# Kernel tuning notes

Measured on AMD Instinct MI355X. Metric: run time of the kernel, lower is better.

## Reference

```python
import jax, jax.numpy as jnp
import numpy as np

D_IN = 2048
D_OUT = 2048
CTX = 2048
N_HEADS = 16
HEAD_DIM = D_OUT // N_HEADS
ROPE_BASE = 10000.0


def precompute_rope(head_dim, context_length, base=ROPE_BASE):
    inv_freq = 1.0 / (base ** (jnp.arange(0, head_dim, 2, dtype=jnp.float32) / head_dim))
    pos = jnp.arange(context_length, dtype=jnp.float32)
    angles = pos[:, None] * inv_freq[None, :]            # (ctx, head_dim/2)
    angles = jnp.concatenate([angles, angles], axis=-1)  # (ctx, head_dim)
    return jnp.cos(angles), jnp.sin(angles)


def compute_rope(x, cos, sin):
    # x: (b, h, s, d)
    s = x.shape[2]
    d = x.shape[3]
    x1, x2 = x[..., : d // 2], x[..., d // 2 :]
    rotated = jnp.concatenate([-x2, x1], axis=-1)
    c = cos[:s][None, None, :, :]
    sn = sin[:s][None, None, :, :]
    return x * c + rotated * sn


def setup_inputs() -> dict:
    key = jax.random.key(0)
    kx, kq, kk, kv, ko = jax.random.split(key, 5)
    scale = 1.0 / np.sqrt(D_IN)
    return {
        "x": jax.random.normal(kx, (2, 2048, D_IN), dtype=jnp.float32),
        "W_query": jax.random.normal(kq, (D_IN, D_OUT), dtype=jnp.float32) * scale,
        "W_key": jax.random.normal(kk, (D_IN, D_OUT), dtype=jnp.float32) * scale,
        "W_value": jax.random.normal(kv, (D_IN, D_OUT), dtype=jnp.float32) * scale,
        "W_out": jax.random.normal(ko, (D_OUT, D_OUT), dtype=jnp.float32) * scale,
    }


def reference(x, W_query, W_key, W_value, W_out):
    b, s, _ = x.shape
    cos, sin = precompute_rope(HEAD_DIM, CTX)

    def split_heads(t):
        return t.reshape(b, s, N_HEADS, HEAD_DIM).transpose(0, 2, 1, 3)  # (b,h,s,d)

    q = split_heads(x @ W_query)
    k = split_heads(x @ W_key)
    v = split_heads(x @ W_value)

    q = compute_rope(q, cos, sin)
    k = compute_rope(k, cos, sin)

    scores = jnp.einsum("bhqd,bhkd->bhqk", q, k) / jnp.sqrt(jnp.float32(HEAD_DIM))
    causal = jnp.tril(jnp.ones((s, s), dtype=bool))
    scores = jnp.where(causal[None, None], scores, -jnp.inf)
    attn = jax.nn.softmax(scores, axis=-1)

    ctx = jnp.einsum("bhqk,bhkd->bhqd", attn, v)
    ctx = ctx.transpose(0, 2, 1, 3).reshape(b, s, D_OUT)
    return ctx @ W_out
```

## Files before the change

kernel.cpp:

```cpp
#include <hip/hip_runtime.h>
#include <hip/hip_bf16.h>

typedef __attribute__((ext_vector_type(8))) short bf16x8;
typedef __attribute__((ext_vector_type(4))) float f32x4;

__device__ inline unsigned short f2bf(float f) {
    unsigned int u = __builtin_bit_cast(unsigned int, f);
    u += 0x7FFFu + ((u >> 16) & 1u);
    return (unsigned short)(u >> 16);
}
__device__ inline float bf2f(unsigned short h) {
    unsigned int u = ((unsigned int)h) << 16;
    return __builtin_bit_cast(float, u);
}


__global__ void k_conv_x(const float* __restrict__ in, unsigned short* __restrict__ out, int n4) {
    int i = blockIdx.x * blockDim.x + threadIdx.x;
    if (i >= n4) return;
    float4 v = ((const float4*)in)[i];
    uint2 o;
    o.x = (unsigned)f2bf(v.x) | ((unsigned)f2bf(v.y) << 16);
    o.y = (unsigned)f2bf(v.z) | ((unsigned)f2bf(v.w) << 16);
    ((uint2*)out)[i] = o;
}

__global__ void k_wT(const float* __restrict__ w0, const float* __restrict__ w1,
                     const float* __restrict__ w2, const float* __restrict__ w3,
                     unsigned short* __restrict__ out) {
    __shared__ float tile[32][33];
    int z = blockIdx.z;
    const float* W = (z == 0) ? w0 : (z == 1) ? w1 : (z == 2) ? w2 : w3;
    unsigned short* O = out + (size_t)z * 2048 * 2048;
    int n0 = blockIdx.x * 32, k0 = blockIdx.y * 32;
    int tx = threadIdx.x & 31, ty = threadIdx.x >> 5;
#pragma unroll
    for (int j = 0; j < 4; ++j)
        tile[ty + j * 8][tx] = W[(size_t)(k0 + ty + j * 8) * 2048 + n0 + tx];
    __syncthreads();
#pragma unroll
    for (int j = 0; j < 4; ++j)
        O[(size_t)(n0 + ty + j * 8) * 2048 + k0 + tx] = f2bf(tile[tx][ty + j * 8]);
}

__global__ void k_rope_table(float* __restrict__ cosT, float* __restrict__ sinT) {
    int t = blockIdx.x * 256 + threadIdx.x;
    int s = t >> 6, i = t & 63;
    float inv = __expf(-((float)i / 64.0f) * 9.210340371976184f);
    float ang = (float)s * inv;
    cosT[t] = cosf(ang);
    sinT[t] = sinf(ang);
}

__global__ void k_rope_apply(unsigned short* qkv, const float* __restrict__ cosT,
                             const float* __restrict__ sinT) {
    int t = blockIdx.x * 256 + threadIdx.x;
    int i = t & 63, h = (t >> 6) & 15, s = (t >> 10) & 2047, b = t >> 21;
    float c = cosT[(s << 6) | i], sn = sinT[(s << 6) | i];
    size_t base = ((size_t)(b * 2048 + s)) * 2048 + h * 128 + i;
    const float SQ = 0.12751742f;
    {
        float a = bf2f(qkv[base]), bb = bf2f(qkv[base + 64]);
        qkv[base]      = f2bf((a * c - bb * sn) * SQ);
        qkv[base + 64] = f2bf((bb * c + a * sn) * SQ);
    }
    {
        size_t kbi = base + (size_t)8388608;
        float a = bf2f(qkv[kbi]), bb = bf2f(qkv[kbi + 64]);
        qkv[kbi]      = f2bf(a * c - bb * sn);
        qkv[kbi + 64] = f2bf(bb * c + a * sn);
    }
}

__global__ void k_vT(const unsigned short* __restrict__ V, unsigned short* __restrict__ VT) {
    __shared__ unsigned short tile[32][33];
    int z = blockIdx.z;
    int s0 = blockIdx.x * 32, d0 = blockIdx.y * 32;
    int b = z >> 4, h = z & 15;
    int tx = threadIdx.x & 31, ty = threadIdx.x >> 5;
#pragma unroll
    for (int j = 0; j < 4; ++j)
        tile[ty + j * 8][tx] =
            V[((size_t)(b * 2048 + s0 + ty + j * 8)) * 2048 + h * 128 + d0 + tx];
    __syncthreads();
#pragma unroll
    for (int j = 0; j < 4; ++j)
        VT[((size_t)(z * 128 + d0 + ty + j * 8)) * 2048 + s0 + tx] = tile[tx][ty + j * 8];
}

template <int OUT_MODE>
__global__ __launch_bounds__(256) void gemm_bt(const unsigned short* __restrict__ A,
                                               const unsigned short* __restrict__ Bt,
                                               void* __restrict__ outp, int M, int N, int K) {
    __shared__ __align__(16) unsigned short As[128 * 64];
    __shared__ __align__(16) unsigned short Bs[128 * 64];
    const int tid = threadIdx.x, w = tid >> 6, l = tid & 63;
    const int m0 = blockIdx.y * 128, n0 = blockIdx.x * 128;
    const int wm = w >> 1, wn = w & 1;
    const int l15 = l & 15, lq = l >> 4;
    f32x4 acc[4][4] = {};
    const int lr = l >> 3, lg = l & 7;
    const int srcg = lg ^ lr;

    const int nkt = K >> 6;
    for (int kt = 0; kt < nkt; ++kt) {
        if (kt) __syncthreads();
#pragma unroll
        for (int i = 0; i < 4; ++i) {
            int r0 = (w * 4 + i) * 8;
            int row = r0 + lr;
            const unsigned short* sa = A + (size_t)(m0 + row) * K + kt * 64 + srcg * 8;
            __builtin_amdgcn_global_load_lds((const void*)sa, (void*)&As[(w * 4 + i) * 512], 16, 0, 0);
            const unsigned short* sb = Bt + (size_t)(n0 + row) * K + kt * 64 + srcg * 8;
            __builtin_amdgcn_global_load_lds((const void*)sb, (void*)&Bs[(w * 4 + i) * 512], 16, 0, 0);
        }
        __syncthreads();
#pragma unroll
        for (int kb = 0; kb < 2; ++kb) {
            bf16x8 af[4], bfr[4];
#pragma unroll
            for (int mi = 0; mi < 4; ++mi) {
                int row = wm * 64 + mi * 16 + l15;
                int g = (kb * 4 + lq) ^ (row & 7);
                af[mi] = *(const bf16x8*)&As[row * 64 + g * 8];
            }
#pragma unroll
            for (int ni = 0; ni < 4; ++ni) {
                int row = wn * 64 + ni * 16 + l15;
                int g = (kb * 4 + lq) ^ (row & 7);
                bfr[ni] = *(const bf16x8*)&Bs[row * 64 + g * 8];
            }
#pragma unroll
            for (int mi = 0; mi < 4; ++mi)
#pragma unroll
                for (int ni = 0; ni < 4; ++ni)
                    acc[mi][ni] = __builtin_amdgcn_mfma_f32_16x16x32_bf16(af[mi], bfr[ni],
                                                                          acc[mi][ni], 0, 0, 0);
        }
    }

    if constexpr (OUT_MODE == 0) {
        int tsel = n0 >> 11, nloc = n0 & 2047;
        unsigned short* op = (unsigned short*)outp + (size_t)tsel * M * 2048;
#pragma unroll
        for (int mi = 0; mi < 4; ++mi)
#pragma unroll
            for (int ni = 0; ni < 4; ++ni)
#pragma unroll
                for (int r = 0; r < 4; ++r) {
                    int row = m0 + wm * 64 + mi * 16 + lq * 4 + r;
                    int col = nloc + wn * 64 + ni * 16 + l15;
                    op[(size_t)row * 2048 + col] = f2bf(acc[mi][ni][r]);
                }
    } else {
        float* op = (float*)outp;
#pragma unroll
        for (int mi = 0; mi < 4; ++mi)
#pragma unroll
            for (int ni = 0; ni < 4; ++ni)
#pragma unroll
                for (int r = 0; r < 4; ++r) {
                    int row = m0 + wm * 64 + mi * 16 + lq * 4 + r;
                    int col = n0 + wn * 64 + ni * 16 + l15;
                    op[(size_t)row * 2048 + col] = acc[mi][ni][r];
                }
    }
}

__global__ __launch_bounds__(512) void k_attn(const unsigned short* __restrict__ Qp,
                                              const unsigned short* __restrict__ Kp,
                                              const unsigned short* __restrict__ VTp,
                                              unsigned short* __restrict__ ctx) {
    __shared__ __align__(16) unsigned short Ks[2][64 * 128];
    __shared__ __align__(16) unsigned short Vs[2][128 * 64];
    __shared__ __align__(16) unsigned short Ps[8][16 * 88];
    const int tid = threadIdx.x, w = tid >> 6, l = tid & 63;
    const int px = blockIdx.x, h = blockIdx.y, b = blockIdx.z;
    const int l15 = l & 15, lq = l >> 4;
    const size_t b2048 = (size_t)b * 2048;
    const int h128 = h * 128;
    const size_t bh128 = (size_t)(b * 16 + h) * 128;

    auto stage = [&](int kv) {
        const int bsel = kv & 1;
        const size_t kvoff = (size_t)kv * 64;
#pragma unroll
        for (int i = 0; i < 2; ++i) {
            int gi = (w * 2 + i) * 64 + l;
            int row = gi >> 4, g = gi & 15;
            int sg = g ^ (row & 7);
            const unsigned short* src = Kp + (b2048 + kvoff + row) * 2048 + h128 + sg * 8;
            __builtin_amdgcn_global_load_lds((const void*)src,
                                             (void*)&Ks[bsel][(w * 2 + i) * 512], 16, 0, 0);
        }
#pragma unroll
        for (int i = 0; i < 2; ++i) {
            int gi = (w * 2 + i) * 64 + l;
            int row = gi >> 3, g = gi & 7;
            int sg = g ^ (row & 7);
            const unsigned short* src = VTp + (bh128 + row) * 2048 + kvoff + sg * 8;
            __builtin_amdgcn_global_load_lds((const void*)src,
                                             (void*)&Vs[bsel][(w * 2 + i) * 512], 16, 0, 0);
        }
    };

    for (int pi = 0; pi < 2; ++pi) {
        const int t = pi ? px : (15 - px);
        const int q0 = t * 128;
        const int wrow0 = q0 + w * 16;

        bf16x8 qf[4];
        {
            const unsigned short* qb = Qp + (b2048 + wrow0 + l15) * 2048 + h128 + lq * 8;
#pragma unroll
            for (int kc = 0; kc < 4; ++kc) qf[kc] = *(const bf16x8*)(qb + kc * 32);
#pragma unroll
            for (int kc = 0; kc < 4; ++kc) asm volatile("" ::"v"(qf[kc]));
        }
        f32x4 O[8] = {};
        float m2[4] = {-1e30f, -1e30f, -1e30f, -1e30f};
        float l2[4] = {0.f, 0.f, 0.f, 0.f};
        const int kvmax = 2 * t + 1;

        stage(0);
        for (int kv = 0; kv <= kvmax; ++kv) {
            const int cur = kv & 1;
            if (kv < kvmax) {
                stage(kv + 1);
                asm volatile("s_waitcnt vmcnt(4)" ::: "memory");
            } else {
                asm volatile("s_waitcnt vmcnt(0)" ::: "memory");
            }
            __builtin_amdgcn_s_barrier();
            __builtin_amdgcn_sched_barrier(0);

            const int kbase = kv * 64;
            if (kbase <= wrow0 + 15) {
                f32x4 S[4] = {};
#pragma unroll
                for (int kc = 0; kc < 4; ++kc)
#pragma unroll
                    for (int nt = 0; nt < 4; ++nt) {
                        int row = nt * 16 + l15;
                        int g = (kc * 4 + lq) ^ (row & 7);
                        bf16x8 kf = *(const bf16x8*)&Ks[cur][row * 128 + g * 8];
                        S[nt] = __builtin_amdgcn_mfma_f32_16x16x32_bf16(qf[kc], kf, S[nt], 0, 0, 0);
                    }

                if (kbase + 63 > wrow0) {
#pragma unroll
                    for (int nt = 0; nt < 4; ++nt) {
                        int col = kbase + nt * 16 + l15;
#pragma unroll
                        for (int r = 0; r < 4; ++r) {
                            int rowg = wrow0 + lq * 4 + r;
                            if (col > rowg) S[nt][r] = -1e30f;
                        }
                    }
                }

#pragma unroll
                for (int r = 0; r < 4; ++r) {
                    float mx = fmaxf(fmaxf(S[0][r], S[1][r]), fmaxf(S[2][r], S[3][r]));
                    mx = fmaxf(mx, __shfl_xor(mx, 1));
                    mx = fmaxf(mx, __shfl_xor(mx, 2));
                    mx = fmaxf(mx, __shfl_xor(mx, 4));
                    mx = fmaxf(mx, __shfl_xor(mx, 8));
                    float mn = fmaxf(m2[r], mx);
                    float sc = __builtin_amdgcn_exp2f(m2[r] - mn);
                    float rs = 0.f;
#pragma unroll
                    for (int nt = 0; nt < 4; ++nt) {
                        float p = __builtin_amdgcn_exp2f(S[nt][r] - mn);
                        S[nt][r] = p;
                        rs += p;
                    }
                    rs += __shfl_xor(rs, 1);
                    rs += __shfl_xor(rs, 2);
                    rs += __shfl_xor(rs, 4);
                    rs += __shfl_xor(rs, 8);
                    l2[r] = l2[r] * sc + rs;
                    m2[r] = mn;
#pragma unroll
                    for (int dt = 0; dt < 8; ++dt) O[dt][r] *= sc;
                }

#pragma unroll
                for (int nt = 0; nt < 4; ++nt)
#pragma unroll
                    for (int r = 0; r < 4; ++r)
                        Ps[w][(lq * 4 + r) * 88 + nt * 16 + l15] = f2bf(S[nt][r]);

                bf16x8 pa[2];
#pragma unroll
                for (int kb = 0; kb < 2; ++kb)
                    pa[kb] = *(const bf16x8*)&Ps[w][l15 * 88 + kb * 32 + lq * 8];

#pragma unroll
                for (int kb = 0; kb < 2; ++kb)
#pragma unroll
                    for (int dt = 0; dt < 8; ++dt) {
                        int row = dt * 16 + l15;
                        int g = (kb * 4 + lq) ^ (row & 7);
                        bf16x8 vf = *(const bf16x8*)&Vs[cur][row * 64 + g * 8];
                        O[dt] = __builtin_amdgcn_mfma_f32_16x16x32_bf16(pa[kb], vf, O[dt], 0, 0, 0);
                    }
            }
            __builtin_amdgcn_sched_barrier(0);
            __builtin_amdgcn_s_barrier();
        }

        float li[4];
#pragma unroll
        for (int r = 0; r < 4; ++r) li[r] = 1.f / l2[r];
#pragma unroll
        for (int dt = 0; dt < 8; ++dt)
#pragma unroll
            for (int r = 0; r < 4; ++r) {
                int rowg = q0 + w * 16 + lq * 4 + r;
                ctx[(b2048 + rowg) * 2048 + h128 + dt * 16 + l15] = f2bf(O[dt][r] * li[r]);
            }
    }
}


extern "C" void kernel_launch(void* const* d_in, const int* in_sizes, int n_in,
                              void* d_out, int out_size, void* d_ws, size_t ws_size,
                              hipStream_t stream) {
    const float* x  = (const float*)d_in[0];
    const float* wq = (const float*)d_in[1];
    const float* wk = (const float*)d_in[2];
    const float* wv = (const float*)d_in[3];
    const float* wo = (const float*)d_in[4];

    char* ws = (char*)d_ws;
    unsigned short* xb  = (unsigned short*)(ws);
    unsigned short* wT  = (unsigned short*)(ws + 16777216);
    unsigned short* qkv = (unsigned short*)(ws + 50331648);
    unsigned short* vT  = (unsigned short*)(ws + 100663296);
    float* cosT = (float*)(ws + 117440512);
    float* sinT = (float*)(ws + 117964800);
    unsigned short* ctx = xb;

    k_conv_x<<<8192, 256, 0, stream>>>(x, xb, 2097152);
    k_wT<<<dim3(64, 64, 4), 256, 0, stream>>>(wq, wk, wv, wo, wT);
    k_rope_table<<<512, 256, 0, stream>>>(cosT, sinT);
    gemm_bt<0><<<dim3(48, 32), 256, 0, stream>>>(xb, wT, (void*)qkv, 4096, 6144, 2048);
    k_rope_apply<<<16384, 256, 0, stream>>>(qkv, cosT, sinT);
    k_vT<<<dim3(64, 4, 32), 256, 0, stream>>>(qkv + 2 * 8388608, vT);
    k_attn<<<dim3(8, 16, 2), 512, 0, stream>>>(qkv, qkv + 8388608, vT, ctx);
    gemm_bt<1><<<dim3(16, 32), 256, 0, stream>>>(ctx, wT + (size_t)3 * 4194304, d_out,
                                                 4096, 2048, 2048);
}
```

Baseline: 283.4 us.

## Rewrite attention with transposed 32x32 MFMA, register P and lazy rescale

The attention kernel switches from 16x16x32 to 32x32x16 MFMAs and computes S^T so each lane owns one query row. This removes the cross-lane shuffle reductions and the LDS round trip for P, since the P fragments are built in registers with a single xor-32 shuffle. The online-softmax rescale now runs only when the max grows by more than a threshold (lazy rescaling). Blocks shrink to 4 waves with 32 rows each, the grid is reordered, and setprio is placed around the MFMA sections. The costs are more registers per lane and a looser max bound that could affect numerics if scores are large.

```diff
diff --git a/kernel.cpp b/kernel.cpp
--- a/kernel.cpp
+++ b/kernel.cpp
@@ -3,6 +3,8 @@
 
 typedef __attribute__((ext_vector_type(8))) short bf16x8;
 typedef __attribute__((ext_vector_type(4))) float f32x4;
+typedef __attribute__((ext_vector_type(16))) float f32x16;
+typedef __attribute__((ext_vector_type(4))) unsigned int u32x4;
 
 __device__ inline unsigned short f2bf(float f) {
     unsigned int u = __builtin_bit_cast(unsigned int, f);
@@ -12,6 +14,9 @@
 __device__ inline float bf2f(unsigned short h) {
     unsigned int u = ((unsigned int)h) << 16;
     return __builtin_bit_cast(float, u);
+}
+__device__ inline unsigned int pkbf(float a, float b) {
+    return (unsigned int)f2bf(a) | ((unsigned int)f2bf(b) << 16);
 }
 
 
@@ -167,59 +172,59 @@
     }
 }
 
-__global__ __launch_bounds__(512) void k_attn(const unsigned short* __restrict__ Qp,
-                                              const unsigned short* __restrict__ Kp,
-                                              const unsigned short* __restrict__ VTp,
-                                              unsigned short* __restrict__ ctx) {
+__global__ __launch_bounds__(256, 2) void k_attn(const unsigned short* __restrict__ Qp,
+                                                 const unsigned short* __restrict__ Kp,
+                                                 const unsigned short* __restrict__ VTp,
+                                                 unsigned short* __restrict__ ctx) {
     __shared__ __align__(16) unsigned short Ks[2][64 * 128];
     __shared__ __align__(16) unsigned short Vs[2][128 * 64];
-    __shared__ __align__(16) unsigned short Ps[8][16 * 88];
     const int tid = threadIdx.x, w = tid >> 6, l = tid & 63;
-    const int px = blockIdx.x, h = blockIdx.y, b = blockIdx.z;
-    const int l15 = l & 15, lq = l >> 4;
+    const int l31 = l & 31, hi = l >> 5;
+    const int x = blockIdx.x, bh = x & 31, pr = x >> 5;
+    const int b = bh >> 4, h = bh & 15;
     const size_t b2048 = (size_t)b * 2048;
     const int h128 = h * 128;
-    const size_t bh128 = (size_t)(b * 16 + h) * 128;
+    const size_t bh128 = (size_t)bh * 128;
 
     auto stage = [&](int kv) {
         const int bsel = kv & 1;
         const size_t kvoff = (size_t)kv * 64;
 #pragma unroll
-        for (int i = 0; i < 2; ++i) {
-            int gi = (w * 2 + i) * 64 + l;
+        for (int i = 0; i < 4; ++i) {
+            int gi = w * 256 + i * 64 + l;
             int row = gi >> 4, g = gi & 15;
             int sg = g ^ (row & 7);
             const unsigned short* src = Kp + (b2048 + kvoff + row) * 2048 + h128 + sg * 8;
             __builtin_amdgcn_global_load_lds((const void*)src,
-                                             (void*)&Ks[bsel][(w * 2 + i) * 512], 16, 0, 0);
-        }
-#pragma unroll
-        for (int i = 0; i < 2; ++i) {
-            int gi = (w * 2 + i) * 64 + l;
+                                             (void*)&Ks[bsel][w * 2048 + i * 512], 16, 0, 0);
+        }
+#pragma unroll
+        for (int i = 0; i < 4; ++i) {
+            int gi = w * 256 + i * 64 + l;
             int row = gi >> 3, g = gi & 7;
             int sg = g ^ (row & 7);
             const unsigned short* src = VTp + (bh128 + row) * 2048 + kvoff + sg * 8;
             __builtin_amdgcn_global_load_lds((const void*)src,
-                                             (void*)&Vs[bsel][(w * 2 + i) * 512], 16, 0, 0);
+                                             (void*)&Vs[bsel][w * 2048 + i * 512], 16, 0, 0);
         }
     };
 
     for (int pi = 0; pi < 2; ++pi) {
-        const int t = pi ? px : (15 - px);
+        const int t = pi ? pr : (15 - pr);
         const int q0 = t * 128;
-        const int wrow0 = q0 + w * 16;
-
-        bf16x8 qf[4];
+        const int wrow0 = q0 + w * 32;
+        const int qg = wrow0 + l31;
+
+        bf16x8 qf[8];
         {
-            const unsigned short* qb = Qp + (b2048 + wrow0 + l15) * 2048 + h128 + lq * 8;
-#pragma unroll
-            for (int kc = 0; kc < 4; ++kc) qf[kc] = *(const bf16x8*)(qb + kc * 32);
-#pragma unroll
-            for (int kc = 0; kc < 4; ++kc) asm volatile("" ::"v"(qf[kc]));
-        }
-        f32x4 O[8] = {};
-        float m2[4] = {-1e30f, -1e30f, -1e30f, -1e30f};
-        float l2[4] = {0.f, 0.f, 0.f, 0.f};
+            const unsigned short* qb = Qp + (b2048 + qg) * 2048 + h128 + hi * 8;
+#pragma unroll
+            for (int ds = 0; ds < 8; ++ds) qf[ds] = *(const bf16x8*)(qb + ds * 16);
+#pragma unroll
+            for (int ds = 0; ds < 8; ++ds) asm volatile("" ::"v"(qf[ds]));
+        }
+        f32x16 Oa[4] = {};
+        float m2 = -1e30f, l2 = 0.f;
         const int kvmax = 2 * t + 1;
 
         stage(0);
@@ -227,98 +232,111 @@
             const int cur = kv & 1;
             if (kv < kvmax) {
                 stage(kv + 1);
-                asm volatile("s_waitcnt vmcnt(4)" ::: "memory");
+                asm volatile("s_waitcnt vmcnt(8)" ::: "memory");
             } else {
                 asm volatile("s_waitcnt vmcnt(0)" ::: "memory");
             }
             __builtin_amdgcn_s_barrier();
             __builtin_amdgcn_sched_barrier(0);
 
-            const int kbase = kv * 64;
-            if (kbase <= wrow0 + 15) {
-                f32x4 S[4] = {};
-#pragma unroll
-                for (int kc = 0; kc < 4; ++kc)
-#pragma unroll
-                    for (int nt = 0; nt < 4; ++nt) {
-                        int row = nt * 16 + l15;
-                        int g = (kc * 4 + lq) ^ (row & 7);
+            const int kvb = kv * 64;
+            if (kvb <= wrow0 + 31) {
+                f32x16 S[2] = {};
+                __builtin_amdgcn_s_setprio(1);
+#pragma unroll
+                for (int ds = 0; ds < 8; ++ds)
+#pragma unroll
+                    for (int st = 0; st < 2; ++st) {
+                        int row = st * 32 + l31;
+                        int g = (ds * 2 + hi) ^ (row & 7);
                         bf16x8 kf = *(const bf16x8*)&Ks[cur][row * 128 + g * 8];
-                        S[nt] = __builtin_amdgcn_mfma_f32_16x16x32_bf16(qf[kc], kf, S[nt], 0, 0, 0);
+                        S[st] = __builtin_amdgcn_mfma_f32_32x32x16_bf16(kf, qf[ds], S[st], 0, 0, 0);
                     }
-
-                if (kbase + 63 > wrow0) {
-#pragma unroll
-                    for (int nt = 0; nt < 4; ++nt) {
-                        int col = kbase + nt * 16 + l15;
-#pragma unroll
-                        for (int r = 0; r < 4; ++r) {
-                            int rowg = wrow0 + lq * 4 + r;
-                            if (col > rowg) S[nt][r] = -1e30f;
+                __builtin_amdgcn_s_setprio(0);
+
+                if (kvb + 63 > wrow0) {
+#pragma unroll
+                    for (int st = 0; st < 2; ++st)
+#pragma unroll
+                        for (int r = 0; r < 16; ++r) {
+                            int kpos = kvb + st * 32 + (r & 3) + 8 * (r >> 2) + 4 * hi;
+                            if (kpos > qg) S[st][r] = -1e30f;
                         }
-                    }
-                }
-
-#pragma unroll
-                for (int r = 0; r < 4; ++r) {
-                    float mx = fmaxf(fmaxf(S[0][r], S[1][r]), fmaxf(S[2][r], S[3][r]));
-                    mx = fmaxf(mx, __shfl_xor(mx, 1));
-                    mx = fmaxf(mx, __shfl_xor(mx, 2));
-                    mx = fmaxf(mx, __shfl_xor(mx, 4));
-                    mx = fmaxf(mx, __shfl_xor(mx, 8));
-                    float mn = fmaxf(m2[r], mx);
-                    float sc = __builtin_amdgcn_exp2f(m2[r] - mn);
-                    float rs = 0.f;
-#pragma unroll
-                    for (int nt = 0; nt < 4; ++nt) {
-                        float p = __builtin_amdgcn_exp2f(S[nt][r] - mn);
-                        S[nt][r] = p;
+                }
+
+                float pmax = -1e30f;
+#pragma unroll
+                for (int st = 0; st < 2; ++st)
+#pragma unroll
+                    for (int r = 0; r < 16; ++r) pmax = fmaxf(pmax, S[st][r]);
+                pmax = fmaxf(pmax, __shfl_xor(pmax, 32));
+                if (__any(pmax > m2 + 8.0f)) {
+                    float mn = fmaxf(m2, pmax);
+                    float sc = __builtin_amdgcn_exp2f(m2 - mn);
+                    m2 = mn;
+                    l2 *= sc;
+#pragma unroll
+                    for (int dt = 0; dt < 4; ++dt)
+#pragma unroll
+                        for (int e = 0; e < 16; ++e) Oa[dt][e] *= sc;
+                }
+                float rs = 0.f;
+#pragma unroll
+                for (int st = 0; st < 2; ++st)
+#pragma unroll
+                    for (int r = 0; r < 16; ++r) {
+                        float p = __builtin_amdgcn_exp2f(S[st][r] - m2);
+                        S[st][r] = p;
                         rs += p;
                     }
-                    rs += __shfl_xor(rs, 1);
-                    rs += __shfl_xor(rs, 2);
-                    rs += __shfl_xor(rs, 4);
-                    rs += __shfl_xor(rs, 8);
-                    l2[r] = l2[r] * sc + rs;
-                    m2[r] = mn;
-#pragma unroll
-                    for (int dt = 0; dt < 8; ++dt) O[dt][r] *= sc;
-                }
-
-#pragma unroll
-                for (int nt = 0; nt < 4; ++nt)
-#pragma unroll
-                    for (int r = 0; r < 4; ++r)
-                        Ps[w][(lq * 4 + r) * 88 + nt * 16 + l15] = f2bf(S[nt][r]);
-
-                bf16x8 pa[2];
-#pragma unroll
-                for (int kb = 0; kb < 2; ++kb)
-                    pa[kb] = *(const bf16x8*)&Ps[w][l15 * 88 + kb * 32 + lq * 8];
-
-#pragma unroll
-                for (int kb = 0; kb < 2; ++kb)
-#pragma unroll
-                    for (int dt = 0; dt < 8; ++dt) {
-                        int row = dt * 16 + l15;
-                        int g = (kb * 4 + lq) ^ (row & 7);
+                rs += __shfl_xor(rs, 32);
+                l2 += rs;
+
+                bf16x8 pfrag[4];
+#pragma unroll
+                for (int ks = 0; ks < 4; ++ks) {
+                    const int st = ks >> 1, base = (ks & 1) * 8;
+                    unsigned int x0 = pkbf(S[st][base + 0], S[st][base + 1]);
+                    unsigned int x1 = pkbf(S[st][base + 2], S[st][base + 3]);
+                    unsigned int y0 = pkbf(S[st][base + 4], S[st][base + 5]);
+                    unsigned int y1 = pkbf(S[st][base + 6], S[st][base + 7]);
+                    unsigned int t0 = hi ? x0 : y0, t1 = hi ? x1 : y1;
+                    t0 = (unsigned int)__shfl_xor((int)t0, 32);
+                    t1 = (unsigned int)__shfl_xor((int)t1, 32);
+                    u32x4 fw;
+                    fw.x = hi ? t0 : x0;
+                    fw.y = hi ? t1 : x1;
+                    fw.z = hi ? y0 : t0;
+                    fw.w = hi ? y1 : t1;
+                    pfrag[ks] = __builtin_bit_cast(bf16x8, fw);
+                }
+
+                __builtin_amdgcn_s_setprio(1);
+#pragma unroll
+                for (int ks = 0; ks < 4; ++ks)
+#pragma unroll
+                    for (int dt = 0; dt < 4; ++dt) {
+                        int row = dt * 32 + l31;
+                        int g = (ks * 2 + hi) ^ (row & 7);
                         bf16x8 vf = *(const bf16x8*)&Vs[cur][row * 64 + g * 8];
-                        O[dt] = __builtin_amdgcn_mfma_f32_16x16x32_bf16(pa[kb], vf, O[dt], 0, 0, 0);
+                        Oa[dt] = __builtin_amdgcn_mfma_f32_32x32x16_bf16(vf, pfrag[ks], Oa[dt], 0, 0, 0);
                     }
+                __builtin_amdgcn_s_setprio(0);
             }
             __builtin_amdgcn_sched_barrier(0);
             __builtin_amdgcn_s_barrier();
         }
 
-        float li[4];
-#pragma unroll
-        for (int r = 0; r < 4; ++r) li[r] = 1.f / l2[r];
-#pragma unroll
-        for (int dt = 0; dt < 8; ++dt)
-#pragma unroll
-            for (int r = 0; r < 4; ++r) {
-                int rowg = q0 + w * 16 + lq * 4 + r;
-                ctx[(b2048 + rowg) * 2048 + h128 + dt * 16 + l15] = f2bf(O[dt][r] * li[r]);
+        float inv = 1.0f / l2;
+        unsigned short* cb = ctx + (b2048 + qg) * 2048 + h128;
+#pragma unroll
+        for (int dt = 0; dt < 4; ++dt)
+#pragma unroll
+            for (int g = 0; g < 4; ++g) {
+                uint2 pv;
+                pv.x = pkbf(Oa[dt][4 * g + 0] * inv, Oa[dt][4 * g + 1] * inv);
+                pv.y = pkbf(Oa[dt][4 * g + 2] * inv, Oa[dt][4 * g + 3] * inv);
+                *(uint2*)(cb + dt * 32 + 8 * g + 4 * hi) = pv;
             }
     }
 }
@@ -348,7 +366,7 @@
     gemm_bt<0><<<dim3(48, 32), 256, 0, stream>>>(xb, wT, (void*)qkv, 4096, 6144, 2048);
     k_rope_apply<<<16384, 256, 0, stream>>>(qkv, cosT, sinT);
     k_vT<<<dim3(64, 4, 32), 256, 0, stream>>>(qkv + 2 * 8388608, vT);
-    k_attn<<<dim3(8, 16, 2), 512, 0, stream>>>(qkv, qkv + 8388608, vT, ctx);
+    k_attn<<<256, 256, 0, stream>>>(qkv, qkv + 8388608, vT, ctx);
     gemm_bt<1><<<dim3(16, 32), 256, 0, stream>>>(ctx, wT + (size_t)3 * 4194304, d_out,
                                                  4096, 2048, 2048);
 }
```

Measured after the change: 269.9 us. -4.8%, faster.
